# Performance work log

Hardware: AMD Instinct MI355X
Metric: run time of the kernel (lower is better)

## Reference

```python
import jax, jax.numpy as jnp
import numpy as np


def setup_inputs() -> dict:
    key = jax.random.key(0)
    k1, k2 = jax.random.split(key)
    x = jax.random.normal(k1, (8192, 128), dtype=jnp.float32)
    y = jax.random.normal(k2, (8192, 128), dtype=jnp.float32)
    return {"x": x, "y": y}


def reference(x, y):
    # Squared pairwise euclidean distances: ||x_i||^2 + ||y_j||^2 - 2 x_i . y_j
    num_pts = x.shape[0]
    x2 = jnp.sum(x * x, axis=1)  # [N]
    y2 = jnp.sum(y * y, axis=1)  # [M]
    dist = x2[:, None] + y2[None, :] - 2.0 * (x @ y.T)  # [N, M]
    dist = jnp.maximum(dist, 0.0)  # matches pow(cdist, 2) up to fp rounding
    in_dist_out = jnp.min(dist, axis=0)   # per-y nearest x, [M]
    out_dist_in = jnp.min(dist, axis=1)   # per-x nearest y, [N]
    loss = jnp.sum(in_dist_out + out_dist_in) / num_pts
    return loss
```

## Files before the change

### kernel.cpp

```cpp
#include <hip/hip_runtime.h>
#include <hip/hip_bf16.h>
#include <stdint.h>


typedef __bf16  bf16x8 __attribute__((ext_vector_type(8)));
typedef float   f32x4  __attribute__((ext_vector_type(4)));

#define NPTS 8192
#define DIM  128
#define KC   256

__device__ __forceinline__ void gload_lds16(const void* gsrc, void* ldst) {
  __builtin_amdgcn_global_load_lds(
      (const __attribute__((address_space(1))) uint32_t*)(uintptr_t)gsrc,
      (__attribute__((address_space(3))) uint32_t*)(uintptr_t)ldst,
      16, 0, 0);
}

__global__ __launch_bounds__(256) void prep_kernel(
    const float* __restrict__ x, const float* __restrict__ y,
    unsigned short* __restrict__ Xc, unsigned short* __restrict__ Yc,
    float* __restrict__ x2, float* __restrict__ y2,
    unsigned int* __restrict__ minx, unsigned int* __restrict__ miny)
{
  const int gt  = blockIdx.x * 256 + threadIdx.x;
  const int row = gt >> 5;
  const int seg = gt & 31;
  const bool isx = row < NPTS;
  const float* src        = isx ? (x  + (size_t)row * DIM) : (y  + (size_t)(row - NPTS) * DIM);
  unsigned short* dst     = isx ? (Xc + (size_t)row * KC)  : (Yc + (size_t)(row - NPTS) * KC);

  f32x4 v = *reinterpret_cast<const f32x4*>(src + seg * 4);
  float sq = v[0]*v[0] + v[1]*v[1] + v[2]*v[2] + v[3]*v[3];
  #pragma unroll
  for (int m = 1; m <= 16; m <<= 1) sq += __shfl_xor(sq, m);
  if (seg == 0) { if (isx) x2[row] = sq; else y2[row - NPTS] = sq; }

  const float scale = isx ? -2.0f : 1.0f;
  unsigned short hb[4], lb[4];
  #pragma unroll
  for (int i = 0; i < 4; ++i) {
    float f = scale * v[i];
    __hip_bfloat16 h = __float2bfloat16(f);
    float hf = __bfloat162float(h);
    __hip_bfloat16 l = __float2bfloat16(f - hf);
    hb[i] = __builtin_bit_cast(unsigned short, h);
    lb[i] = __builtin_bit_cast(unsigned short, l);
  }
  *reinterpret_cast<ushort4*>(dst + seg * 4)       = make_ushort4(hb[0], hb[1], hb[2], hb[3]);
  *reinterpret_cast<ushort4*>(dst + 128 + seg * 4) = make_ushort4(lb[0], lb[1], lb[2], lb[3]);

  if (gt < NPTS)          minx[gt]        = 0x7F800000u;
  else if (gt < 2 * NPTS) miny[gt - NPTS] = 0x7F800000u;
}

__global__ __launch_bounds__(512, 2) void chamfer_gemm(
    const unsigned short* __restrict__ Xc, const unsigned short* __restrict__ Yc,
    const float* __restrict__ x2, const float* __restrict__ y2,
    unsigned int* __restrict__ minx, unsigned int* __restrict__ miny)
{
  __shared__ alignas(16) unsigned short As[2][256 * 64];
  __shared__ alignas(16) unsigned short Bs[2][256 * 64];
  float* colminLDS = (float*)&As[0][0];
  float* rowminLDS = (float*)&As[0][0] + 512;

  const int tid  = threadIdx.x;
  const int lane = tid & 63;
  const int w    = tid >> 6;
  const int wr   = w >> 2;
  const int wc   = w & 3;

  const int bid   = blockIdx.x;
  const int xcd   = bid & 7;
  const int local = bid >> 3;
  const int bi    = xcd * 4 + ((local >> 3) & 3);
  const int bj    = ((local >> 5) << 3) + (local & 7);

  const int r64  = tid >> 3;
  const int kgrp = (tid & 7) ^ (r64 & 7);
  const unsigned short* Abase = Xc + (size_t)(bi * 256 + r64) * KC + kgrp * 8;
  const unsigned short* Bbase = Yc + (size_t)(bj * 256 + r64) * KC + kgrp * 8;

  auto STAGE = [&](int buf, int kt) {
    const unsigned short* Asrc = Abase + kt * 64;
    const unsigned short* Bsrc = Bbase + kt * 64;
    char* Ad = (char*)&As[buf][0] + w * 1024;
    char* Bd = (char*)&Bs[buf][0] + w * 1024;
    #pragma unroll
    for (int l = 0; l < 4; ++l) {
      gload_lds16(Asrc + (size_t)l * 64 * KC, Ad + l * 8192);
      gload_lds16(Bsrc + (size_t)l * 64 * KC, Bd + l * 8192);
    }
  };

  f32x4 acc[8][4];
  {
    f32x4 xv[8]; float yv[4];
    #pragma unroll
    for (int mi = 0; mi < 8; ++mi)
      xv[mi] = *reinterpret_cast<const f32x4*>(x2 + bi * 256 + wr * 128 + mi * 16 + ((lane >> 4) << 2));
    #pragma unroll
    for (int ni = 0; ni < 4; ++ni)
      yv[ni] = y2[bj * 256 + wc * 64 + ni * 16 + (lane & 15)];
    #pragma unroll
    for (int mi = 0; mi < 8; ++mi)
      #pragma unroll
      for (int ni = 0; ni < 4; ++ni)
        #pragma unroll
        for (int r = 0; r < 4; ++r)
          acc[mi][ni][r] = xv[mi][r] + yv[ni];
  }

  STAGE(0, 0);
  __syncthreads();

  #pragma unroll
  for (int kt = 0; kt < 4; ++kt) {
    if (kt < 3) STAGE((kt + 1) & 1, kt + 1);
    const char* Ab = (const char*)&As[kt & 1][0];
    const char* Bb = (const char*)&Bs[kt & 1][0];

    bf16x8 b[4][2];
    #pragma unroll
    for (int ni = 0; ni < 4; ++ni) {
      const int col = wc * 64 + ni * 16 + (lane & 15);
      const int swz = (col & 7) << 4;
      #pragma unroll
      for (int ks = 0; ks < 2; ++ks) {
        const int ofs = (ks * 64 + ((lane >> 4) << 4)) ^ swz;
        b[ni][ks] = *reinterpret_cast<const bf16x8*>(Bb + col * 128 + ofs);
      }
    }
    #pragma unroll
    for (int mi = 0; mi < 8; ++mi) {
      const int rowl = wr * 128 + mi * 16 + (lane & 15);
      const int swz  = (rowl & 7) << 4;
      const bf16x8 a0 = *reinterpret_cast<const bf16x8*>(Ab + rowl * 128 + ((  0 + ((lane >> 4) << 4)) ^ swz));
      const bf16x8 a1 = *reinterpret_cast<const bf16x8*>(Ab + rowl * 128 + (( 64 + ((lane >> 4) << 4)) ^ swz));
      #pragma unroll
      for (int ni = 0; ni < 4; ++ni) {
        acc[mi][ni] = __builtin_amdgcn_mfma_f32_16x16x32_bf16(a0, b[ni][0], acc[mi][ni], 0, 0, 0);
        acc[mi][ni] = __builtin_amdgcn_mfma_f32_16x16x32_bf16(a1, b[ni][1], acc[mi][ni], 0, 0, 0);
      }
    }
    __syncthreads();
  }

  float cm[4];
  #pragma unroll
  for (int ni = 0; ni < 4; ++ni) {
    float m = 3.0e38f;
    #pragma unroll
    for (int mi = 0; mi < 8; ++mi)
      #pragma unroll
      for (int r = 0; r < 4; ++r)
        m = fminf(m, acc[mi][ni][r]);
    cm[ni] = m;
  }
  {
    const bool hb0 = (lane & 16) != 0;
    float s0 = hb0 ? cm[0] : cm[2];
    float s1 = hb0 ? cm[1] : cm[3];
    float r0 = __shfl_xor(s0, 16);
    float r1 = __shfl_xor(s1, 16);
    float t0 = fminf(hb0 ? cm[2] : cm[0], r0);
    float t1 = fminf(hb0 ? cm[3] : cm[1], r1);
    const bool hb1 = (lane & 32) != 0;
    float s  = hb1 ? t0 : t1;
    float rr = __shfl_xor(s, 32);
    float cfin = fminf(hb1 ? t1 : t0, rr);
    const int ni = (hb0 ? 2 : 0) + (hb1 ? 1 : 0);
    colminLDS[wr * 256 + wc * 64 + ni * 16 + (lane & 15)] = cfin;
  }

  float rm[32];
  #pragma unroll
  for (int mi = 0; mi < 8; ++mi)
    #pragma unroll
    for (int r = 0; r < 4; ++r)
      rm[mi * 4 + r] = fminf(fminf(acc[mi][0][r], acc[mi][1][r]),
                             fminf(acc[mi][2][r], acc[mi][3][r]));
  #pragma unroll
  for (int b2 = 0; b2 < 4; ++b2) {
    const int  half = 16 >> b2;
    const bool up   = (lane >> b2) & 1;
    #pragma unroll
    for (int i = 0; i < half; ++i) {
      float snd = up ? rm[i] : rm[i + half];
      float rcv = __shfl_xor(snd, 1 << b2);
      rm[i] = fminf(up ? rm[i + half] : rm[i], rcv);
    }
  }
  {
    const int base = ((lane & 1) << 4) | ((lane & 2) << 2) | (lane & 4) | ((lane & 8) >> 2);
    #pragma unroll
    for (int e = 0; e < 2; ++e) {
      const int idx = base | e;
      const int row_local = wr * 128 + (idx >> 2) * 16 + ((lane >> 4) << 2) + (idx & 3);
      rowminLDS[wc * 256 + row_local] = rm[e];
    }
  }
  __syncthreads();

  if (tid < 256) {
    float c = fminf(colminLDS[tid], colminLDS[256 + tid]);
    atomicMin(&miny[bj * 256 + tid], __float_as_uint(fmaxf(c, 0.f)));
  } else {
    const int r = tid - 256;
    float v = fminf(fminf(rowminLDS[r], rowminLDS[256 + r]),
                    fminf(rowminLDS[512 + r], rowminLDS[768 + r]));
    atomicMin(&minx[bi * 256 + r], __float_as_uint(fmaxf(v, 0.f)));
  }
}

__global__ __launch_bounds__(256) void finalize_kernel(
    const unsigned int* __restrict__ minx, const unsigned int* __restrict__ miny,
    float* __restrict__ out)
{
  const f32x4* mx = (const f32x4*)minx;
  const f32x4* my = (const f32x4*)miny;
  float s = 0.f;
  for (int i = threadIdx.x; i < NPTS / 4; i += 256) {
    f32x4 a = mx[i], b = my[i];
    s += (a[0] + a[1] + a[2] + a[3]) + (b[0] + b[1] + b[2] + b[3]);
  }
  #pragma unroll
  for (int m = 32; m >= 1; m >>= 1) s += __shfl_xor(s, m);
  __shared__ float partial[4];
  if ((threadIdx.x & 63) == 0) partial[threadIdx.x >> 6] = s;
  __syncthreads();
  if (threadIdx.x == 0)
    out[0] = (partial[0] + partial[1] + partial[2] + partial[3]) * (1.0f / (float)NPTS);
}

extern "C" void kernel_launch(void* const* d_in, const int* in_sizes, int n_in,
                              void* d_out, int out_size, void* d_ws, size_t ws_size,
                              hipStream_t stream) {
  (void)in_sizes; (void)n_in; (void)out_size; (void)ws_size;
  const float* x = (const float*)d_in[0];
  const float* y = (const float*)d_in[1];
  char* ws = (char*)d_ws;

  unsigned short* Xc  = (unsigned short*)(ws);
  unsigned short* Yc  = (unsigned short*)(ws + 4194304);
  float*          x2  = (float*)(ws + 8388608);
  float*          y2  = (float*)(ws + 8421376);
  unsigned int*   mnx = (unsigned int*)(ws + 8454144);
  unsigned int*   mny = (unsigned int*)(ws + 8486912);
  float*          out = (float*)d_out;

  prep_kernel<<<2048, 256, 0, stream>>>(x, y, Xc, Yc, x2, y2, mnx, mny);
  chamfer_gemm<<<1024, 512, 0, stream>>>(Xc, Yc, x2, y2, mnx, mny);
  finalize_kernel<<<1, 256, 0, stream>>>(mnx, mny, out);
}
```

Before: 99.77 us.

## Make GEMM blocks persistent over four column tiles and fuse the final reduction

The GEMM grid shrinks from 1024 to 256 blocks. Each block keeps its X row tile and walks four Y column tiles, with a continuous double-buffered prefetch that runs across tile boundaries and raises wave priority around the MFMA section. The separate finalize kernel is removed: the last block to finish, found through an atomic counter, sums the minima and writes the loss. The aim is to cut launch overhead and the per-tile pipeline fill and drain. In exchange, 256 blocks at two blocks per CU may leave the device partly occupied and serialize each block's epilogue atomics with its compute.

```diff
diff --git a/kernel.cpp b/kernel.cpp
--- a/kernel.cpp
+++ b/kernel.cpp
@@ -21,7 +21,8 @@
     const float* __restrict__ x, const float* __restrict__ y,
     unsigned short* __restrict__ Xc, unsigned short* __restrict__ Yc,
     float* __restrict__ x2, float* __restrict__ y2,
-    unsigned int* __restrict__ minx, unsigned int* __restrict__ miny)
+    unsigned int* __restrict__ minx, unsigned int* __restrict__ miny,
+    unsigned int* __restrict__ cnt)
 {
   const int gt  = blockIdx.x * 256 + threadIdx.x;
   const int row = gt >> 5;
@@ -52,17 +53,21 @@
 
   if (gt < NPTS)          minx[gt]        = 0x7F800000u;
   else if (gt < 2 * NPTS) miny[gt - NPTS] = 0x7F800000u;
+  if (gt == 0) cnt[0] = 0u;
 }
 
 __global__ __launch_bounds__(512, 2) void chamfer_gemm(
     const unsigned short* __restrict__ Xc, const unsigned short* __restrict__ Yc,
     const float* __restrict__ x2, const float* __restrict__ y2,
-    unsigned int* __restrict__ minx, unsigned int* __restrict__ miny)
+    unsigned int* __restrict__ minx, unsigned int* __restrict__ miny,
+    unsigned int* __restrict__ cnt, float* __restrict__ out)
 {
   __shared__ alignas(16) unsigned short As[2][256 * 64];
   __shared__ alignas(16) unsigned short Bs[2][256 * 64];
-  float* colminLDS = (float*)&As[0][0];
-  float* rowminLDS = (float*)&As[0][0] + 512;
+  __shared__ float colminLDS[2 * 256];
+  __shared__ float rowminLDS[4 * 256];
+  __shared__ float redLDS[8];
+  __shared__ unsigned int lastFlag;
 
   const int tid  = threadIdx.x;
   const int lane = tid & 63;
@@ -70,20 +75,20 @@
   const int wr   = w >> 2;
   const int wc   = w & 3;
 
-  const int bid   = blockIdx.x;
-  const int xcd   = bid & 7;
-  const int local = bid >> 3;
-  const int bi    = xcd * 4 + ((local >> 3) & 3);
-  const int bj    = ((local >> 5) << 3) + (local & 7);
+  const int b   = blockIdx.x;
+  const int I   = (b & 7) >> 2;
+  const int J   = b & 3;
+  const int wi  = b >> 3;
+  const int bi  = I * 16 + (wi >> 1);
+  const int bj0 = J * 8 + (wi & 1) * 4;
 
   const int r64  = tid >> 3;
   const int kgrp = (tid & 7) ^ (r64 & 7);
   const unsigned short* Abase = Xc + (size_t)(bi * 256 + r64) * KC + kgrp * 8;
-  const unsigned short* Bbase = Yc + (size_t)(bj * 256 + r64) * KC + kgrp * 8;
-
-  auto STAGE = [&](int buf, int kt) {
-    const unsigned short* Asrc = Abase + kt * 64;
-    const unsigned short* Bsrc = Bbase + kt * 64;
+
+  auto STAGE = [&](int buf, int nt, int nkt) {
+    const unsigned short* Asrc = Abase + nkt * 64;
+    const unsigned short* Bsrc = Yc + (size_t)((bj0 + nt) * 256 + r64) * KC + kgrp * 8 + nkt * 64;
     char* Ad = (char*)&As[buf][0] + w * 1024;
     char* Bd = (char*)&Bs[buf][0] + w * 1024;
     #pragma unroll
@@ -93,144 +98,164 @@
     }
   };
 
-  f32x4 acc[8][4];
-  {
-    f32x4 xv[8]; float yv[4];
+  STAGE(0, 0, 0);
+
+  for (int t = 0; t < 4; ++t) {
+    const int bj = bj0 + t;
+
+    f32x4 acc[8][4];
+    {
+      f32x4 xv[8]; float yv[4];
+      #pragma unroll
+      for (int mi = 0; mi < 8; ++mi)
+        xv[mi] = *reinterpret_cast<const f32x4*>(x2 + bi * 256 + wr * 128 + mi * 16 + ((lane >> 4) << 2));
+      #pragma unroll
+      for (int ni = 0; ni < 4; ++ni)
+        yv[ni] = y2[bj * 256 + wc * 64 + ni * 16 + (lane & 15)];
+      #pragma unroll
+      for (int mi = 0; mi < 8; ++mi)
+        #pragma unroll
+        for (int ni = 0; ni < 4; ++ni)
+          #pragma unroll
+          for (int r = 0; r < 4; ++r)
+            acc[mi][ni][r] = xv[mi][r] + yv[ni];
+    }
+
+    #pragma unroll
+    for (int kt = 0; kt < 4; ++kt) {
+      const int step = t * 4 + kt;
+      const int buf  = step & 1;
+
+      asm volatile("s_waitcnt vmcnt(0)" ::: "memory");
+      __builtin_amdgcn_s_barrier();
+      __builtin_amdgcn_sched_barrier(0);
+
+      if (step < 15) {
+        const int ns = step + 1;
+        STAGE(ns & 1, ns >> 2, ns & 3);
+      }
+
+      const char* Ab = (const char*)&As[buf][0];
+      const char* Bb = (const char*)&Bs[buf][0];
+
+      __builtin_amdgcn_s_setprio(1);
+      bf16x8 bfr[4][2];
+      #pragma unroll
+      for (int ni = 0; ni < 4; ++ni) {
+        const int col = wc * 64 + ni * 16 + (lane & 15);
+        const int swz = (col & 7) << 4;
+        #pragma unroll
+        for (int ks = 0; ks < 2; ++ks) {
+          const int ofs = (ks * 64 + ((lane >> 4) << 4)) ^ swz;
+          bfr[ni][ks] = *reinterpret_cast<const bf16x8*>(Bb + col * 128 + ofs);
+        }
+      }
+      #pragma unroll
+      for (int mi = 0; mi < 8; ++mi) {
+        const int rowl = wr * 128 + mi * 16 + (lane & 15);
+        const int swz  = (rowl & 7) << 4;
+        const bf16x8 a0 = *reinterpret_cast<const bf16x8*>(Ab + rowl * 128 + ((  0 + ((lane >> 4) << 4)) ^ swz));
+        const bf16x8 a1 = *reinterpret_cast<const bf16x8*>(Ab + rowl * 128 + (( 64 + ((lane >> 4) << 4)) ^ swz));
+        #pragma unroll
+        for (int ni = 0; ni < 4; ++ni) {
+          acc[mi][ni] = __builtin_amdgcn_mfma_f32_16x16x32_bf16(a0, bfr[ni][0], acc[mi][ni], 0, 0, 0);
+          acc[mi][ni] = __builtin_amdgcn_mfma_f32_16x16x32_bf16(a1, bfr[ni][1], acc[mi][ni], 0, 0, 0);
+        }
+      }
+      __builtin_amdgcn_s_setprio(0);
+    }
+
+    float cm[4];
+    #pragma unroll
+    for (int ni = 0; ni < 4; ++ni) {
+      float m = 3.0e38f;
+      #pragma unroll
+      for (int mi = 0; mi < 8; ++mi)
+        #pragma unroll
+        for (int r = 0; r < 4; ++r)
+          m = fminf(m, acc[mi][ni][r]);
+      cm[ni] = m;
+    }
+    {
+      const bool hb0 = (lane & 16) != 0;
+      float s0 = hb0 ? cm[0] : cm[2];
+      float s1 = hb0 ? cm[1] : cm[3];
+      float r0 = __shfl_xor(s0, 16);
+      float r1 = __shfl_xor(s1, 16);
+      float t0 = fminf(hb0 ? cm[2] : cm[0], r0);
+      float t1 = fminf(hb0 ? cm[3] : cm[1], r1);
+      const bool hb1 = (lane & 32) != 0;
+      float s  = hb1 ? t0 : t1;
+      float rr = __shfl_xor(s, 32);
+      float cfin = fminf(hb1 ? t1 : t0, rr);
+      const int ni = (hb0 ? 2 : 0) + (hb1 ? 1 : 0);
+      colminLDS[wr * 256 + wc * 64 + ni * 16 + (lane & 15)] = cfin;
+    }
+
+    float rm[32];
     #pragma unroll
     for (int mi = 0; mi < 8; ++mi)
-      xv[mi] = *reinterpret_cast<const f32x4*>(x2 + bi * 256 + wr * 128 + mi * 16 + ((lane >> 4) << 2));
-    #pragma unroll
-    for (int ni = 0; ni < 4; ++ni)
-      yv[ni] = y2[bj * 256 + wc * 64 + ni * 16 + (lane & 15)];
-    #pragma unroll
-    for (int mi = 0; mi < 8; ++mi)
-      #pragma unroll
-      for (int ni = 0; ni < 4; ++ni)
-        #pragma unroll
-        for (int r = 0; r < 4; ++r)
-          acc[mi][ni][r] = xv[mi][r] + yv[ni];
-  }
-
-  STAGE(0, 0);
+      #pragma unroll
+      for (int r = 0; r < 4; ++r)
+        rm[mi * 4 + r] = fminf(fminf(acc[mi][0][r], acc[mi][1][r]),
+                               fminf(acc[mi][2][r], acc[mi][3][r]));
+    #pragma unroll
+    for (int b2 = 0; b2 < 4; ++b2) {
+      const int  half = 16 >> b2;
+      const bool up   = (lane >> b2) & 1;
+      #pragma unroll
+      for (int i = 0; i < half; ++i) {
+        float snd = up ? rm[i] : rm[i + half];
+        float rcv = __shfl_xor(snd, 1 << b2);
+        rm[i] = fminf(up ? rm[i + half] : rm[i], rcv);
+      }
+    }
+    {
+      const int base = ((lane & 1) << 4) | ((lane & 2) << 2) | (lane & 4) | ((lane & 8) >> 2);
+      #pragma unroll
+      for (int e = 0; e < 2; ++e) {
+        const int idx = base | e;
+        const int row_local = wr * 128 + (idx >> 2) * 16 + ((lane >> 4) << 2) + (idx & 3);
+        rowminLDS[wc * 256 + row_local] = rm[e];
+      }
+    }
+    __syncthreads();
+
+    if (tid < 256) {
+      float c = fminf(colminLDS[tid], colminLDS[256 + tid]);
+      atomicMin(&miny[bj * 256 + tid], __float_as_uint(fmaxf(c, 0.f)));
+    } else {
+      const int r = tid - 256;
+      float v = fminf(fminf(rowminLDS[r], rowminLDS[256 + r]),
+                      fminf(rowminLDS[512 + r], rowminLDS[768 + r]));
+      atomicMin(&minx[bi * 256 + r], __float_as_uint(fmaxf(v, 0.f)));
+    }
+  }
+
   __syncthreads();
-
-  #pragma unroll
-  for (int kt = 0; kt < 4; ++kt) {
-    if (kt < 3) STAGE((kt + 1) & 1, kt + 1);
-    const char* Ab = (const char*)&As[kt & 1][0];
-    const char* Bb = (const char*)&Bs[kt & 1][0];
-
-    bf16x8 b[4][2];
-    #pragma unroll
-    for (int ni = 0; ni < 4; ++ni) {
-      const int col = wc * 64 + ni * 16 + (lane & 15);
-      const int swz = (col & 7) << 4;
-      #pragma unroll
-      for (int ks = 0; ks < 2; ++ks) {
-        const int ofs = (ks * 64 + ((lane >> 4) << 4)) ^ swz;
-        b[ni][ks] = *reinterpret_cast<const bf16x8*>(Bb + col * 128 + ofs);
-      }
-    }
-    #pragma unroll
-    for (int mi = 0; mi < 8; ++mi) {
-      const int rowl = wr * 128 + mi * 16 + (lane & 15);
-      const int swz  = (rowl & 7) << 4;
-      const bf16x8 a0 = *reinterpret_cast<const bf16x8*>(Ab + rowl * 128 + ((  0 + ((lane >> 4) << 4)) ^ swz));
-      const bf16x8 a1 = *reinterpret_cast<const bf16x8*>(Ab + rowl * 128 + (( 64 + ((lane >> 4) << 4)) ^ swz));
-      #pragma unroll
-      for (int ni = 0; ni < 4; ++ni) {
-        acc[mi][ni] = __builtin_amdgcn_mfma_f32_16x16x32_bf16(a0, b[ni][0], acc[mi][ni], 0, 0, 0);
-        acc[mi][ni] = __builtin_amdgcn_mfma_f32_16x16x32_bf16(a1, b[ni][1], acc[mi][ni], 0, 0, 0);
-      }
-    }
+  if (tid == 0) {
+    __threadfence();
+    unsigned int old = __hip_atomic_fetch_add(cnt, 1u, __ATOMIC_ACQ_REL, __HIP_MEMORY_SCOPE_AGENT);
+    lastFlag = (old == 255u) ? 1u : 0u;
+  }
+  __syncthreads();
+  if (lastFlag) {
+    float s = 0.f;
+    for (int i = tid; i < NPTS; i += 512) {
+      s += __uint_as_float(__hip_atomic_load(&minx[i], __ATOMIC_RELAXED, __HIP_MEMORY_SCOPE_AGENT));
+      s += __uint_as_float(__hip_atomic_load(&miny[i], __ATOMIC_RELAXED, __HIP_MEMORY_SCOPE_AGENT));
+    }
+    #pragma unroll
+    for (int m = 32; m >= 1; m >>= 1) s += __shfl_xor(s, m);
+    if (lane == 0) redLDS[w] = s;
     __syncthreads();
-  }
-
-  float cm[4];
-  #pragma unroll
-  for (int ni = 0; ni < 4; ++ni) {
-    float m = 3.0e38f;
-    #pragma unroll
-    for (int mi = 0; mi < 8; ++mi)
-      #pragma unroll
-      for (int r = 0; r < 4; ++r)
-        m = fminf(m, acc[mi][ni][r]);
-    cm[ni] = m;
-  }
-  {
-    const bool hb0 = (lane & 16) != 0;
-    float s0 = hb0 ? cm[0] : cm[2];
-    float s1 = hb0 ? cm[1] : cm[3];
-    float r0 = __shfl_xor(s0, 16);
-    float r1 = __shfl_xor(s1, 16);
-    float t0 = fminf(hb0 ? cm[2] : cm[0], r0);
-    float t1 = fminf(hb0 ? cm[3] : cm[1], r1);
-    const bool hb1 = (lane & 32) != 0;
-    float s  = hb1 ? t0 : t1;
-    float rr = __shfl_xor(s, 32);
-    float cfin = fminf(hb1 ? t1 : t0, rr);
-    const int ni = (hb0 ? 2 : 0) + (hb1 ? 1 : 0);
-    colminLDS[wr * 256 + wc * 64 + ni * 16 + (lane & 15)] = cfin;
-  }
-
-  float rm[32];
-  #pragma unroll
-  for (int mi = 0; mi < 8; ++mi)
-    #pragma unroll
-    for (int r = 0; r < 4; ++r)
-      rm[mi * 4 + r] = fminf(fminf(acc[mi][0][r], acc[mi][1][r]),
-                             fminf(acc[mi][2][r], acc[mi][3][r]));
-  #pragma unroll
-  for (int b2 = 0; b2 < 4; ++b2) {
-    const int  half = 16 >> b2;
-    const bool up   = (lane >> b2) & 1;
-    #pragma unroll
-    for (int i = 0; i < half; ++i) {
-      float snd = up ? rm[i] : rm[i + half];
-      float rcv = __shfl_xor(snd, 1 << b2);
-      rm[i] = fminf(up ? rm[i + half] : rm[i], rcv);
-    }
-  }
-  {
-    const int base = ((lane & 1) << 4) | ((lane & 2) << 2) | (lane & 4) | ((lane & 8) >> 2);
-    #pragma unroll
-    for (int e = 0; e < 2; ++e) {
-      const int idx = base | e;
-      const int row_local = wr * 128 + (idx >> 2) * 16 + ((lane >> 4) << 2) + (idx & 3);
-      rowminLDS[wc * 256 + row_local] = rm[e];
-    }
-  }
-  __syncthreads();
-
-  if (tid < 256) {
-    float c = fminf(colminLDS[tid], colminLDS[256 + tid]);
-    atomicMin(&miny[bj * 256 + tid], __float_as_uint(fmaxf(c, 0.f)));
-  } else {
-    const int r = tid - 256;
-    float v = fminf(fminf(rowminLDS[r], rowminLDS[256 + r]),
-                    fminf(rowminLDS[512 + r], rowminLDS[768 + r]));
-    atomicMin(&minx[bi * 256 + r], __float_as_uint(fmaxf(v, 0.f)));
-  }
-}
-
-__global__ __launch_bounds__(256) void finalize_kernel(
-    const unsigned int* __restrict__ minx, const unsigned int* __restrict__ miny,
-    float* __restrict__ out)
-{
-  const f32x4* mx = (const f32x4*)minx;
-  const f32x4* my = (const f32x4*)miny;
-  float s = 0.f;
-  for (int i = threadIdx.x; i < NPTS / 4; i += 256) {
-    f32x4 a = mx[i], b = my[i];
-    s += (a[0] + a[1] + a[2] + a[3]) + (b[0] + b[1] + b[2] + b[3]);
-  }
-  #pragma unroll
-  for (int m = 32; m >= 1; m >>= 1) s += __shfl_xor(s, m);
-  __shared__ float partial[4];
-  if ((threadIdx.x & 63) == 0) partial[threadIdx.x >> 6] = s;
-  __syncthreads();
-  if (threadIdx.x == 0)
-    out[0] = (partial[0] + partial[1] + partial[2] + partial[3]) * (1.0f / (float)NPTS);
+    if (tid == 0) {
+      float tsum = 0.f;
+      #pragma unroll
+      for (int i = 0; i < 8; ++i) tsum += redLDS[i];
+      out[0] = tsum * (1.0f / (float)NPTS);
+    }
+  }
 }
 
 extern "C" void kernel_launch(void* const* d_in, const int* in_sizes, int n_in,
@@ -247,9 +272,9 @@
   float*          y2  = (float*)(ws + 8421376);
   unsigned int*   mnx = (unsigned int*)(ws + 8454144);
   unsigned int*   mny = (unsigned int*)(ws + 8486912);
+  unsigned int*   cnt = (unsigned int*)(ws + 8519680);
   float*          out = (float*)d_out;
 
-  prep_kernel<<<2048, 256, 0, stream>>>(x, y, Xc, Yc, x2, y2, mnx, mny);
-  chamfer_gemm<<<1024, 512, 0, stream>>>(Xc, Yc, x2, y2, mnx, mny);
-  finalize_kernel<<<1, 256, 0, stream>>>(mnx, mny, out);
-}
+  prep_kernel<<<2048, 256, 0, stream>>>(x, y, Xc, Yc, x2, y2, mnx, mny, cnt);
+  chamfer_gemm<<<256, 512, 0, stream>>>(Xc, Yc, x2, y2, mnx, mny, cnt, out);
+}
```

Measured after the change: 108.8 us. 9.1% more time.
